# Kernel tuning notes

Measured on AMD Instinct MI355X. Metric: run time of the kernel, lower is better.

## Reference

```python
import jax, jax.numpy as jnp
import numpy as np
from jax import lax

INPUT_DIM = 256
STATE_DIM = 512
B, T = 128, 1024


def setup_inputs() -> dict:
    key = jax.random.key(0)
    ks = jax.random.split(key, 9)
    s = STATE_DIM
    i = INPUT_DIM
    # Linear(state_dim, state_dim, bias=False), weight scaled by 0.2 as in __init__
    lim_s = 1.0 / np.sqrt(s)
    lim_i = 1.0 / np.sqrt(i)
    A0_w = jax.random.uniform(ks[0], (s, s), jnp.float32, -lim_s, lim_s) * 0.2
    A1_w = jax.random.uniform(ks[1], (s, s), jnp.float32, -lim_s, lim_s) * 0.2
    B0_w = jax.random.uniform(ks[2], (s, i), jnp.float32, -lim_i, lim_i)
    B0_b = jax.random.uniform(ks[3], (s,), jnp.float32, -lim_i, lim_i)
    B1_w = jax.random.uniform(ks[4], (s, i), jnp.float32, -lim_i, lim_i)
    B1_b = jax.random.uniform(ks[5], (s,), jnp.float32, -lim_i, lim_i)
    gate_w = jax.random.uniform(ks[6], (s, i), jnp.float32, -lim_i, lim_i)
    gate_b = jax.random.uniform(ks[7], (s,), jnp.float32, -lim_i, lim_i)
    x_seq = jax.random.normal(ks[8], (B, T, i), jnp.float32)
    s0 = jnp.zeros((B, s), jnp.float32)
    alpha = jnp.float32(0.5)
    return {
        "x_seq": x_seq, "s0": s0,
        "A0_w": A0_w, "B0_w": B0_w, "B0_b": B0_b,
        "A1_w": A1_w, "B1_w": B1_w, "B1_b": B1_b,
        "gate_w": gate_w, "gate_b": gate_b,
        "alpha": alpha, "z": 1,
    }


def reference(x_seq, s0, A0_w, B0_w, B0_b, A1_w, B1_w, B1_b, gate_w, gate_b, alpha, z):
    # Precompute all input projections in one batched GEMM each: [B, T, S]
    bx0 = jnp.einsum('bti,si->bts', x_seq, B0_w) + B0_b
    bx1 = jnp.einsum('bti,si->bts', x_seq, B1_w) + B1_b
    gx = jax.nn.sigmoid(jnp.einsum('bti,si->bts', x_seq, gate_w) + gate_b)

    def step_fn(s, inputs):
        b0_t, b1_t, g_t = inputs  # each [B, S]
        f0 = jnp.tanh(s @ A0_w.T + b0_t)
        if z == 0:
            f = f0
        else:
            f1 = jnp.tanh(s @ A1_w.T + b1_t)
            f = (1.0 - alpha) * f0 + alpha * f1
        s_new = g_t * f + (1.0 - g_t) * s
        return s_new, s_new

    # scan over time: move T to leading axis
    xs = (jnp.swapaxes(bx0, 0, 1), jnp.swapaxes(bx1, 0, 1), jnp.swapaxes(gx, 0, 1))
    _, states = lax.scan(step_fn, s0, xs)  # states: [T, B, S]
    # prepend s0 -> [B, T+1, S]
    return jnp.concatenate([s0[:, None, :], jnp.swapaxes(states, 0, 1)], axis=1)
```

## Files before the change

### kernel.cpp

```cpp
#include <hip/hip_runtime.h>
#include <hip/hip_bf16.h>
#include <math.h>

typedef __attribute__((ext_vector_type(8))) short bf16x8;
typedef __attribute__((ext_vector_type(4))) float f32x4;
typedef __attribute__((ext_vector_type(4))) int i32x4;

#define TT 1024
#define BB 128
#define II 256
#define SS 512
#define OUT_T 1025
#define OUT_BSTRIDE ((size_t)OUT_T * SS)

static __device__ __forceinline__ unsigned short f2bf(float f) {
  union { float f; unsigned int u; } v; v.f = f;
  unsigned int r = v.u + 0x7fffu + ((v.u >> 16) & 1u);
  return (unsigned short)(r >> 16);
}
static __device__ __forceinline__ float bf2f(unsigned short h) {
  union { unsigned int u; float f; } v; v.u = ((unsigned int)h) << 16;
  return v.f;
}
static __device__ __forceinline__ bf16x8 pack8(const float* p) {
  float4 a = *(const float4*)p;
  float4 b = *(const float4*)(p + 4);
  bf16x8 r;
  r[0]=(short)f2bf(a.x); r[1]=(short)f2bf(a.y); r[2]=(short)f2bf(a.z); r[3]=(short)f2bf(a.w);
  r[4]=(short)f2bf(b.x); r[5]=(short)f2bf(b.y); r[6]=(short)f2bf(b.z); r[7]=(short)f2bf(b.w);
  return r;
}
static __device__ __forceinline__ float fast_tanh(float x) {
  float x2 = fminf(x * 2.8853900817779268f, 88.0f);
  float e = __builtin_amdgcn_exp2f(x2);
  return (e - 1.0f) * __builtin_amdgcn_rcpf(e + 1.0f);
}

static __device__ __forceinline__ i32x4 ld_coh_b128_issue(const void* p) {
  i32x4 r;
  asm volatile("global_load_dwordx4 %0, %1, off sc0 sc1" : "=v"(r) : "v"(p) : "memory");
  return r;
}
static __device__ __forceinline__ unsigned int ld_coh_b32(const void* p) {
  unsigned int r;
  asm volatile("global_load_dword %0, %1, off sc0 sc1\n\ts_waitcnt vmcnt(0)"
               : "=v"(r) : "v"(p) : "memory");
  return r;
}
static __device__ __forceinline__ void st_coh_b128(void* p, i32x4 v) {
  asm volatile("global_store_dwordx4 %0, %1, off sc0 sc1" :: "v"(p), "v"(v) : "memory");
}
static __device__ __forceinline__ void st_coh_b32(void* p, unsigned int v) {
  asm volatile("global_store_dword %0, %1, off sc0 sc1" :: "v"(p), "v"(v) : "memory");
}
static __device__ __forceinline__ void waitcnt_vm0() {
  asm volatile("s_waitcnt vmcnt(0)" ::: "memory");
}

__global__ __launch_bounds__(256) void proj_kernel(
    const float* __restrict__ x,
    const float* __restrict__ B0w, const float* __restrict__ B0b,
    const float* __restrict__ B1w, const float* __restrict__ B1b,
    const float* __restrict__ Gw,  const float* __restrict__ Gb,
    unsigned short* __restrict__ proj)
{
  __shared__ unsigned short Ab[64 * 40];
  __shared__ unsigned short Bb[64 * 40];
  int bid = blockIdx.x;
  int nb = bid % 24, mb = bid / 24;
  int m0 = mb * 64, n0 = nb * 64;
  const float* Wp; const float* bp; bool isgate = false;
  if (n0 < 512)       { Wp = B0w + (size_t)n0 * II;          bp = B0b + n0; }
  else if (n0 < 1024) { Wp = B1w + (size_t)(n0 - 512) * II;  bp = B1b + (n0 - 512); }
  else                { Wp = Gw  + (size_t)(n0 - 1024) * II; bp = Gb + (n0 - 1024); isgate = true; }

  int tid = threadIdx.x;
  int lane = tid & 63, wid = tid >> 6;
  int r = tid >> 2, c = tid & 3;
  int mt0 = (wid >> 1) * 2, nt0 = (wid & 1) * 2;

  f32x4 acc[2][2] = {};
  for (int k0 = 0; k0 < II; k0 += 32) {
    __syncthreads();
    *(bf16x8*)&Ab[r * 40 + c * 8] = pack8(x  + (size_t)(m0 + r) * II + k0 + c * 8);
    *(bf16x8*)&Bb[r * 40 + c * 8] = pack8(Wp + (size_t)r * II       + k0 + c * 8);
    __syncthreads();
    bf16x8 af[2], bf[2];
#pragma unroll
    for (int mi = 0; mi < 2; ++mi)
      af[mi] = *(const bf16x8*)&Ab[((mt0 + mi) * 16 + (lane & 15)) * 40 + 8 * (lane >> 4)];
#pragma unroll
    for (int ni = 0; ni < 2; ++ni)
      bf[ni] = *(const bf16x8*)&Bb[((nt0 + ni) * 16 + (lane & 15)) * 40 + 8 * (lane >> 4)];
#pragma unroll
    for (int mi = 0; mi < 2; ++mi)
#pragma unroll
      for (int ni = 0; ni < 2; ++ni)
        acc[mi][ni] = __builtin_amdgcn_mfma_f32_16x16x32_bf16(af[mi], bf[ni], acc[mi][ni], 0, 0, 0);
  }
#pragma unroll
  for (int mi = 0; mi < 2; ++mi)
#pragma unroll
    for (int ni = 0; ni < 2; ++ni)
#pragma unroll
      for (int q = 0; q < 4; ++q) {
        int m  = m0 + (mt0 + mi) * 16 + (lane >> 4) * 4 + q;
        int nl = (nt0 + ni) * 16 + (lane & 15);
        int b = m >> 10, t = m & 1023;
        float v = acc[mi][ni][q] + bp[nl];
        if (isgate) v = 1.0f / (1.0f + expf(-v));
        proj[((size_t)t * BB + b) * 1536 + n0 + nl] = f2bf(v);
      }
}

__global__ __launch_bounds__(256, 1) void recur_kernel(
    const float* __restrict__ s0,
    const float* __restrict__ A0w, const float* __restrict__ A1w,
    const unsigned short* __restrict__ proj,
    const float* __restrict__ alpha_p, const int* __restrict__ z_p,
    unsigned short* state_bf,
    unsigned int* flags,
    float* __restrict__ out)
{
  __shared__ unsigned short Ss[16 * 520];

  int tid = threadIdx.x, lane = tid & 63, wid = tid >> 6;
  int g = blockIdx.x & 7, j = blockIdx.x >> 3;
  int b0 = g * 16, c0 = j * 64;
  int lane15 = lane & 15, kslot = lane >> 4;
  int rowbase = kslot * 4;
  int colw = c0 + wid * 16 + lane15;
  float alpha = *alpha_p; int z = *z_p;
  float om_a = 1.0f - alpha;

  bf16x8 Af0[16], Af1[16];
#pragma unroll
  for (int kk = 0; kk < 16; ++kk) {
    int k0 = kk * 32 + kslot * 8;
    Af0[kk] = pack8(A0w + (size_t)colw * SS + k0);
    Af1[kk] = pack8(A1w + (size_t)colw * SS + k0);
  }

#pragma unroll
  for (int c2 = 0; c2 < 4; ++c2) {
    int e = tid + 256 * c2; int rr = e >> 6, kc = e & 63;
    *(bf16x8*)&Ss[rr * 520 + kc * 8] = pack8(s0 + (size_t)(b0 + rr) * SS + kc * 8);
  }
  if (j == 0) {
#pragma unroll
    for (int c2 = 0; c2 < 4; ++c2) {
      int e = tid + 256 * c2; int rr = e >> 6, kc = e & 63;
      const float* sp = s0 + (size_t)(b0 + rr) * SS + kc * 8;
      float* op = out + (size_t)(b0 + rr) * OUT_BSTRIDE + kc * 8;
      *(float4*)op = *(const float4*)sp;
      *(float4*)(op + 4) = *(const float4*)(sp + 4);
    }
  }
  float sprev[4];
#pragma unroll
  for (int q = 0; q < 4; ++q)
    sprev[q] = s0[(size_t)(b0 + rowbase + q) * SS + colw];

  const unsigned short* pj[4];
  unsigned short pb0[4], pb1[4], pg[4];
#pragma unroll
  for (int q = 0; q < 4; ++q) {
    pj[q] = proj + (size_t)(b0 + rowbase + q) * 1536 + colw;
    pb0[q] = pj[q][0]; pb1[q] = pj[q][512]; pg[q] = pj[q][1024];
  }

  __syncthreads();

  for (int t = 0; t < TT; ++t) {
    f32x4 acc0 = {0.f,0.f,0.f,0.f}, acc1 = {0.f,0.f,0.f,0.f};
    const unsigned short* sb = &Ss[lane15 * 520 + kslot * 8];
#pragma unroll
    for (int kk = 0; kk < 16; ++kk) {
      bf16x8 af = *(const bf16x8*)(sb + kk * 32);
      acc0 = __builtin_amdgcn_mfma_f32_16x16x32_bf16(af, Af0[kk], acc0, 0, 0, 0);
      acc1 = __builtin_amdgcn_mfma_f32_16x16x32_bf16(af, Af1[kk], acc1, 0, 0, 0);
    }
    __syncthreads();

    float sn[4];
#pragma unroll
    for (int q = 0; q < 4; ++q) {
      float f0 = fast_tanh(acc0[q] + bf2f(pb0[q]));
      float f;
      if (z != 0) {
        float f1 = fast_tanh(acc1[q] + bf2f(pb1[q]));
        f = om_a * f0 + alpha * f1;
      } else {
        f = f0;
      }
      float gg = bf2f(pg[q]);
      sn[q] = gg * f + (1.0f - gg) * sprev[q];
      sprev[q] = sn[q];
      Ss[(rowbase + q) * 520 + colw] = f2bf(sn[q]);
    }
    __syncthreads();

    unsigned short* snext = state_bf + (size_t)((t + 1) & 1) * BB * SS;
    if (tid < 128) {
      int row = tid >> 3, ch = tid & 7;
      i32x4 v = *(const i32x4*)&Ss[row * 520 + c0 + ch * 8];
      st_coh_b128(snext + (size_t)(b0 + row) * SS + c0 + ch * 8, v);
      waitcnt_vm0();
    }
    __syncthreads();
    if (tid == 0) st_coh_b32(flags + g * 8 + j, (unsigned int)(t + 1));

#pragma unroll
    for (int q = 0; q < 4; ++q)
      out[(size_t)(b0 + rowbase + q) * OUT_BSTRIDE + (size_t)(t + 1) * SS + colw] = sn[q];
    if (t + 1 < TT) {
#pragma unroll
      for (int q = 0; q < 4; ++q) {
        pj[q] += (size_t)BB * 1536;
        pb0[q] = pj[q][0]; pb1[q] = pj[q][512]; pg[q] = pj[q][1024];
      }
      if (wid == 0 && lane < 8) {
        const unsigned int* fp = flags + g * 8 + lane;
        while (ld_coh_b32(fp) < (unsigned int)(t + 1)) {}
      }
      __syncthreads();
      i32x4 v[4];
#pragma unroll
      for (int c2 = 0; c2 < 4; ++c2) {
        int e = tid + 256 * c2; int rr = e >> 6, kc = e & 63;
        v[c2] = ld_coh_b128_issue(snext + (size_t)(b0 + rr) * SS + kc * 8);
      }
      waitcnt_vm0();
#pragma unroll
      for (int c2 = 0; c2 < 4; ++c2) {
        int e = tid + 256 * c2; int rr = e >> 6, kc = e & 63;
        *(bf16x8*)&Ss[rr * 520 + kc * 8] = *(bf16x8*)&v[c2];
      }
      __syncthreads();
    }
  }
}

extern "C" void kernel_launch(void* const* d_in, const int* in_sizes, int n_in,
                              void* d_out, int out_size, void* d_ws, size_t ws_size,
                              hipStream_t stream) {
  const float* x   = (const float*)d_in[0];
  const float* s0  = (const float*)d_in[1];
  const float* A0w = (const float*)d_in[2];
  const float* B0w = (const float*)d_in[3];
  const float* B0b = (const float*)d_in[4];
  const float* A1w = (const float*)d_in[5];
  const float* B1w = (const float*)d_in[6];
  const float* B1b = (const float*)d_in[7];
  const float* Gw  = (const float*)d_in[8];
  const float* Gb  = (const float*)d_in[9];
  const float* alp = (const float*)d_in[10];
  const int*   zp  = (const int*)d_in[11];
  float* out = (float*)d_out;

  char* ws = (char*)d_ws;
  size_t proj_bytes  = (size_t)BB * TT * 1536 * 2;
  size_t state_off   = proj_bytes;
  size_t state_bytes = (size_t)2 * BB * SS * 2;
  size_t flag_off    = state_off + state_bytes;
  unsigned short* proj     = (unsigned short*)(ws);
  unsigned short* state_bf = (unsigned short*)(ws + state_off);
  unsigned int*   flags    = (unsigned int*)(ws + flag_off);

  hipMemsetAsync(flags, 0, 64 * sizeof(unsigned int), stream);

  proj_kernel<<<dim3((131072 / 64) * (1536 / 64)), dim3(256), 0, stream>>>(
      x, B0w, B0b, B1w, B1b, Gw, Gb, proj);

  recur_kernel<<<dim3(64), dim3(256), 0, stream>>>(
      s0, A0w, A1w, proj, alp, zp, state_bf, flags, out);
}
```

Before: 3.026 ms.

## Interleave two batch halves in recurrence and tile projection over all outputs per block

The recurrent kernel now runs on 32 blocks, and each block owns two 16-row batch groups. It alternates between them so that one group's state exchange and flag wait overlap the other group's MFMA compute. It also splits each accumulator into even and odd chains to shorten MFMA dependency chains, and writes the transposed MFMA output as vectorized float4 and 64-bit stores. The projection kernel keeps a 64-row x tile resident in LDS and loops over all 24 output tiles, so x is not reloaded once per tile. The cost is halving the recurrence parallelism and putting more serial work on each block.

```diff
diff --git a/kernel.cpp b/kernel.cpp
--- a/kernel.cpp
+++ b/kernel.cpp
@@ -5,6 +5,8 @@
 typedef __attribute__((ext_vector_type(8))) short bf16x8;
 typedef __attribute__((ext_vector_type(4))) float f32x4;
 typedef __attribute__((ext_vector_type(4))) int i32x4;
+typedef __attribute__((ext_vector_type(2))) int i32x2;
+typedef __attribute__((ext_vector_type(2))) unsigned int u32x2;
 
 #define TT 1024
 #define BB 128
@@ -30,6 +32,11 @@
   r[4]=(short)f2bf(b.x); r[5]=(short)f2bf(b.y); r[6]=(short)f2bf(b.z); r[7]=(short)f2bf(b.w);
   return r;
 }
+static __device__ __forceinline__ float bfat(u32x2 v, int q) {
+  unsigned int u = (q < 2) ? v[0] : v[1];
+  u = (q & 1) ? (u >> 16) : (u & 0xffffu);
+  return bf2f((unsigned short)u);
+}
 static __device__ __forceinline__ float fast_tanh(float x) {
   float x2 = fminf(x * 2.8853900817779268f, 88.0f);
   float e = __builtin_amdgcn_exp2f(x2);
@@ -47,8 +54,8 @@
                : "=v"(r) : "v"(p) : "memory");
   return r;
 }
-static __device__ __forceinline__ void st_coh_b128(void* p, i32x4 v) {
-  asm volatile("global_store_dwordx4 %0, %1, off sc0 sc1" :: "v"(p), "v"(v) : "memory");
+static __device__ __forceinline__ void st_coh_b64(void* p, i32x2 v) {
+  asm volatile("global_store_dwordx2 %0, %1, off sc0 sc1" :: "v"(p), "v"(v) : "memory");
 }
 static __device__ __forceinline__ void st_coh_b32(void* p, unsigned int v) {
   asm volatile("global_store_dword %0, %1, off sc0 sc1" :: "v"(p), "v"(v) : "memory");
@@ -64,53 +71,61 @@
     const float* __restrict__ Gw,  const float* __restrict__ Gb,
     unsigned short* __restrict__ proj)
 {
-  __shared__ unsigned short Ab[64 * 40];
-  __shared__ unsigned short Bb[64 * 40];
-  int bid = blockIdx.x;
-  int nb = bid % 24, mb = bid / 24;
-  int m0 = mb * 64, n0 = nb * 64;
-  const float* Wp; const float* bp; bool isgate = false;
-  if (n0 < 512)       { Wp = B0w + (size_t)n0 * II;          bp = B0b + n0; }
-  else if (n0 < 1024) { Wp = B1w + (size_t)(n0 - 512) * II;  bp = B1b + (n0 - 512); }
-  else                { Wp = Gw  + (size_t)(n0 - 1024) * II; bp = Gb + (n0 - 1024); isgate = true; }
-
-  int tid = threadIdx.x;
-  int lane = tid & 63, wid = tid >> 6;
-  int r = tid >> 2, c = tid & 3;
+  __shared__ unsigned short Xs[64 * 264];
+  __shared__ unsigned short Ws[64 * 40];
+
+  int m0 = blockIdx.x * 64;
+  int tid = threadIdx.x, lane = tid & 63, wid = tid >> 6;
+  int lane15 = lane & 15, kslot = lane >> 4;
   int mt0 = (wid >> 1) * 2, nt0 = (wid & 1) * 2;
-
-  f32x4 acc[2][2] = {};
-  for (int k0 = 0; k0 < II; k0 += 32) {
-    __syncthreads();
-    *(bf16x8*)&Ab[r * 40 + c * 8] = pack8(x  + (size_t)(m0 + r) * II + k0 + c * 8);
-    *(bf16x8*)&Bb[r * 40 + c * 8] = pack8(Wp + (size_t)r * II       + k0 + c * 8);
-    __syncthreads();
-    bf16x8 af[2], bf[2];
+  int sr = tid >> 2, sc = tid & 3;
+
+#pragma unroll
+  for (int it = 0; it < 8; ++it) {
+    int task = tid + 256 * it; int r = task >> 5, c = task & 31;
+    *(bf16x8*)&Xs[r * 264 + c * 8] = pack8(x + (size_t)(m0 + r) * II + c * 8);
+  }
+  __syncthreads();
+
+  for (int nt = 0; nt < 24; ++nt) {
+    int n0 = nt * 64;
+    const float* Wp; const float* bp; bool isgate = false;
+    if (n0 < 512)       { Wp = B0w + (size_t)n0 * II;          bp = B0b + n0; }
+    else if (n0 < 1024) { Wp = B1w + (size_t)(n0 - 512) * II;  bp = B1b + (n0 - 512); }
+    else                { Wp = Gw  + (size_t)(n0 - 1024) * II; bp = Gb + (n0 - 1024); isgate = true; }
+
+    f32x4 acc[2][2] = {};
+    for (int k0 = 0; k0 < II; k0 += 32) {
+      __syncthreads();
+      *(bf16x8*)&Ws[sr * 40 + sc * 8] = pack8(Wp + (size_t)sr * II + k0 + sc * 8);
+      __syncthreads();
+      bf16x8 af[2], bf[2];
+#pragma unroll
+      for (int mi = 0; mi < 2; ++mi)
+        af[mi] = *(const bf16x8*)&Xs[((mt0 + mi) * 16 + lane15) * 264 + k0 + 8 * kslot];
+#pragma unroll
+      for (int ni = 0; ni < 2; ++ni)
+        bf[ni] = *(const bf16x8*)&Ws[((nt0 + ni) * 16 + lane15) * 40 + 8 * kslot];
+#pragma unroll
+      for (int mi = 0; mi < 2; ++mi)
+#pragma unroll
+        for (int ni = 0; ni < 2; ++ni)
+          acc[mi][ni] = __builtin_amdgcn_mfma_f32_16x16x32_bf16(af[mi], bf[ni], acc[mi][ni], 0, 0, 0);
+    }
 #pragma unroll
     for (int mi = 0; mi < 2; ++mi)
-      af[mi] = *(const bf16x8*)&Ab[((mt0 + mi) * 16 + (lane & 15)) * 40 + 8 * (lane >> 4)];
-#pragma unroll
-    for (int ni = 0; ni < 2; ++ni)
-      bf[ni] = *(const bf16x8*)&Bb[((nt0 + ni) * 16 + (lane & 15)) * 40 + 8 * (lane >> 4)];
-#pragma unroll
-    for (int mi = 0; mi < 2; ++mi)
 #pragma unroll
       for (int ni = 0; ni < 2; ++ni)
-        acc[mi][ni] = __builtin_amdgcn_mfma_f32_16x16x32_bf16(af[mi], bf[ni], acc[mi][ni], 0, 0, 0);
-  }
-#pragma unroll
-  for (int mi = 0; mi < 2; ++mi)
-#pragma unroll
-    for (int ni = 0; ni < 2; ++ni)
-#pragma unroll
-      for (int q = 0; q < 4; ++q) {
-        int m  = m0 + (mt0 + mi) * 16 + (lane >> 4) * 4 + q;
-        int nl = (nt0 + ni) * 16 + (lane & 15);
-        int b = m >> 10, t = m & 1023;
-        float v = acc[mi][ni][q] + bp[nl];
-        if (isgate) v = 1.0f / (1.0f + expf(-v));
-        proj[((size_t)t * BB + b) * 1536 + n0 + nl] = f2bf(v);
-      }
+#pragma unroll
+        for (int q = 0; q < 4; ++q) {
+          int m  = m0 + (mt0 + mi) * 16 + kslot * 4 + q;
+          int nl = (nt0 + ni) * 16 + lane15;
+          int b = m >> 10, t = m & 1023;
+          float v = acc[mi][ni][q] + bp[nl];
+          if (isgate) v = 1.0f / (1.0f + expf(-v));
+          proj[((size_t)t * BB + b) * 1536 + n0 + nl] = f2bf(v);
+        }
+  }
 }
 
 __global__ __launch_bounds__(256, 1) void recur_kernel(
@@ -122,16 +137,18 @@
     unsigned int* flags,
     float* __restrict__ out)
 {
-  __shared__ unsigned short Ss[16 * 520];
+  __shared__ unsigned short SsA[16 * 520];
+  __shared__ unsigned short SsB[16 * 520];
 
   int tid = threadIdx.x, lane = tid & 63, wid = tid >> 6;
-  int g = blockIdx.x & 7, j = blockIdx.x >> 3;
-  int b0 = g * 16, c0 = j * 64;
+  int g = blockIdx.x & 3, j = blockIdx.x >> 2;
+  int bA = g * 32, bB = g * 32 + 16;
+  int c0 = j * 64;
   int lane15 = lane & 15, kslot = lane >> 4;
-  int rowbase = kslot * 4;
   int colw = c0 + wid * 16 + lane15;
-  float alpha = *alpha_p; int z = *z_p;
-  float om_a = 1.0f - alpha;
+  int ccb  = c0 + wid * 16 + kslot * 4;
+  int rowA = bA + lane15, rowB = bB + lane15;
+  float alpha = *alpha_p; int z = *z_p; float om_a = 1.0f - alpha;
 
   bf16x8 Af0[16], Af1[16];
 #pragma unroll
@@ -144,97 +161,158 @@
 #pragma unroll
   for (int c2 = 0; c2 < 4; ++c2) {
     int e = tid + 256 * c2; int rr = e >> 6, kc = e & 63;
-    *(bf16x8*)&Ss[rr * 520 + kc * 8] = pack8(s0 + (size_t)(b0 + rr) * SS + kc * 8);
+    *(bf16x8*)&SsA[rr * 520 + kc * 8] = pack8(s0 + (size_t)(bA + rr) * SS + kc * 8);
+    *(bf16x8*)&SsB[rr * 520 + kc * 8] = pack8(s0 + (size_t)(bB + rr) * SS + kc * 8);
   }
   if (j == 0) {
 #pragma unroll
-    for (int c2 = 0; c2 < 4; ++c2) {
-      int e = tid + 256 * c2; int rr = e >> 6, kc = e & 63;
-      const float* sp = s0 + (size_t)(b0 + rr) * SS + kc * 8;
-      float* op = out + (size_t)(b0 + rr) * OUT_BSTRIDE + kc * 8;
-      *(float4*)op = *(const float4*)sp;
-      *(float4*)(op + 4) = *(const float4*)(sp + 4);
-    }
-  }
-  float sprev[4];
-#pragma unroll
-  for (int q = 0; q < 4; ++q)
-    sprev[q] = s0[(size_t)(b0 + rowbase + q) * SS + colw];
-
-  const unsigned short* pj[4];
-  unsigned short pb0[4], pb1[4], pg[4];
-#pragma unroll
-  for (int q = 0; q < 4; ++q) {
-    pj[q] = proj + (size_t)(b0 + rowbase + q) * 1536 + colw;
-    pb0[q] = pj[q][0]; pb1[q] = pj[q][512]; pg[q] = pj[q][1024];
-  }
+    for (int it = 0; it < 16; ++it) {
+      int task = tid + 256 * it;
+      int rr = task >> 7, f4 = task & 127;
+      *(float4*)(out + (size_t)(bA + rr) * OUT_BSTRIDE + f4 * 4) =
+          *(const float4*)(s0 + (size_t)(bA + rr) * SS + f4 * 4);
+    }
+  }
+  float4 spA4 = *(const float4*)(s0 + (size_t)rowA * SS + ccb);
+  float4 spB4 = *(const float4*)(s0 + (size_t)rowB * SS + ccb);
+  float sprevA[4] = {spA4.x, spA4.y, spA4.z, spA4.w};
+  float sprevB[4] = {spB4.x, spB4.y, spB4.z, spB4.w};
+
+  const unsigned short* ppA = proj + (size_t)rowA * 1536 + ccb;
+  const unsigned short* ppB = proj + (size_t)rowB * 1536 + ccb;
+  u32x2 pA0 = *(const u32x2*)(ppA);
+  u32x2 pA1 = *(const u32x2*)(ppA + 512);
+  u32x2 pAg = *(const u32x2*)(ppA + 1024);
+  u32x2 pB0 = *(const u32x2*)(ppB);
+  u32x2 pB1 = *(const u32x2*)(ppB + 512);
+  u32x2 pBg = *(const u32x2*)(ppB + 1024);
+
+  unsigned int* flagA = flags + g * 8;
+  unsigned int* flagB = flags + 32 + g * 8;
 
   __syncthreads();
 
   for (int t = 0; t < TT; ++t) {
-    f32x4 acc0 = {0.f,0.f,0.f,0.f}, acc1 = {0.f,0.f,0.f,0.f};
-    const unsigned short* sb = &Ss[lane15 * 520 + kslot * 8];
-#pragma unroll
-    for (int kk = 0; kk < 16; ++kk) {
-      bf16x8 af = *(const bf16x8*)(sb + kk * 32);
-      acc0 = __builtin_amdgcn_mfma_f32_16x16x32_bf16(af, Af0[kk], acc0, 0, 0, 0);
-      acc1 = __builtin_amdgcn_mfma_f32_16x16x32_bf16(af, Af1[kk], acc1, 0, 0, 0);
-    }
-    __syncthreads();
-
-    float sn[4];
-#pragma unroll
-    for (int q = 0; q < 4; ++q) {
-      float f0 = fast_tanh(acc0[q] + bf2f(pb0[q]));
-      float f;
-      if (z != 0) {
-        float f1 = fast_tanh(acc1[q] + bf2f(pb1[q]));
-        f = om_a * f0 + alpha * f1;
-      } else {
-        f = f0;
-      }
-      float gg = bf2f(pg[q]);
-      sn[q] = gg * f + (1.0f - gg) * sprev[q];
-      sprev[q] = sn[q];
-      Ss[(rowbase + q) * 520 + colw] = f2bf(sn[q]);
-    }
-    __syncthreads();
-
     unsigned short* snext = state_bf + (size_t)((t + 1) & 1) * BB * SS;
-    if (tid < 128) {
-      int row = tid >> 3, ch = tid & 7;
-      i32x4 v = *(const i32x4*)&Ss[row * 520 + c0 + ch * 8];
-      st_coh_b128(snext + (size_t)(b0 + row) * SS + c0 + ch * 8, v);
+
+    {
+      f32x4 a0e = {}, a0o = {}, a1e = {}, a1o = {};
+      const unsigned short* sb = &SsA[lane15 * 520 + kslot * 8];
+#pragma unroll
+      for (int kk = 0; kk < 16; kk += 2) {
+        bf16x8 f0 = *(const bf16x8*)(sb + kk * 32);
+        bf16x8 f1 = *(const bf16x8*)(sb + (kk + 1) * 32);
+        a0e = __builtin_amdgcn_mfma_f32_16x16x32_bf16(Af0[kk],     f0, a0e, 0, 0, 0);
+        a1e = __builtin_amdgcn_mfma_f32_16x16x32_bf16(Af1[kk],     f0, a1e, 0, 0, 0);
+        a0o = __builtin_amdgcn_mfma_f32_16x16x32_bf16(Af0[kk + 1], f1, a0o, 0, 0, 0);
+        a1o = __builtin_amdgcn_mfma_f32_16x16x32_bf16(Af1[kk + 1], f1, a1o, 0, 0, 0);
+      }
+      float snA[4];
+#pragma unroll
+      for (int q = 0; q < 4; ++q) {
+        float f0 = fast_tanh((a0e[q] + a0o[q]) + bfat(pA0, q));
+        float f;
+        if (z != 0) {
+          float f1 = fast_tanh((a1e[q] + a1o[q]) + bfat(pA1, q));
+          f = om_a * f0 + alpha * f1;
+        } else f = f0;
+        float gg = bfat(pAg, q);
+        snA[q] = gg * f + (1.0f - gg) * sprevA[q];
+        sprevA[q] = snA[q];
+      }
+      float4 o4 = {snA[0], snA[1], snA[2], snA[3]};
+      *(float4*)(out + (size_t)rowA * OUT_BSTRIDE + (size_t)(t + 1) * SS + ccb) = o4;
+      i32x2 w;
+      w[0] = (int)(((unsigned)f2bf(snA[0])) | (((unsigned)f2bf(snA[1])) << 16));
+      w[1] = (int)(((unsigned)f2bf(snA[2])) | (((unsigned)f2bf(snA[3])) << 16));
+      st_coh_b64(snext + (size_t)rowA * SS + ccb, w);
       waitcnt_vm0();
-    }
-    __syncthreads();
-    if (tid == 0) st_coh_b32(flags + g * 8 + j, (unsigned int)(t + 1));
-
-#pragma unroll
-    for (int q = 0; q < 4; ++q)
-      out[(size_t)(b0 + rowbase + q) * OUT_BSTRIDE + (size_t)(t + 1) * SS + colw] = sn[q];
-    if (t + 1 < TT) {
-#pragma unroll
-      for (int q = 0; q < 4; ++q) {
-        pj[q] += (size_t)BB * 1536;
-        pb0[q] = pj[q][0]; pb1[q] = pj[q][512]; pg[q] = pj[q][1024];
-      }
-      if (wid == 0 && lane < 8) {
-        const unsigned int* fp = flags + g * 8 + lane;
-        while (ld_coh_b32(fp) < (unsigned int)(t + 1)) {}
-      }
-      __syncthreads();
+      __syncthreads();
+      if (tid == 0) st_coh_b32(flagA + j, (unsigned int)(t + 1));
+      if (t + 1 < TT) {
+        ppA += (size_t)BB * 1536;
+        pA0 = *(const u32x2*)(ppA);
+        pA1 = *(const u32x2*)(ppA + 512);
+        pAg = *(const u32x2*)(ppA + 1024);
+      }
+    }
+
+    if (t > 0) {
+      if (tid < 8) { while (ld_coh_b32(flagB + tid) < (unsigned int)t) {} }
+      __syncthreads();
+      const unsigned short* sbg = state_bf + (size_t)(t & 1) * BB * SS + (size_t)bB * SS;
       i32x4 v[4];
 #pragma unroll
       for (int c2 = 0; c2 < 4; ++c2) {
         int e = tid + 256 * c2; int rr = e >> 6, kc = e & 63;
-        v[c2] = ld_coh_b128_issue(snext + (size_t)(b0 + rr) * SS + kc * 8);
+        v[c2] = ld_coh_b128_issue(sbg + rr * SS + kc * 8);
       }
       waitcnt_vm0();
 #pragma unroll
       for (int c2 = 0; c2 < 4; ++c2) {
         int e = tid + 256 * c2; int rr = e >> 6, kc = e & 63;
-        *(bf16x8*)&Ss[rr * 520 + kc * 8] = *(bf16x8*)&v[c2];
+        *(bf16x8*)&SsB[rr * 520 + kc * 8] = *(bf16x8*)&v[c2];
+      }
+      __syncthreads();
+    }
+
+    {
+      f32x4 a0e = {}, a0o = {}, a1e = {}, a1o = {};
+      const unsigned short* sb = &SsB[lane15 * 520 + kslot * 8];
+#pragma unroll
+      for (int kk = 0; kk < 16; kk += 2) {
+        bf16x8 f0 = *(const bf16x8*)(sb + kk * 32);
+        bf16x8 f1 = *(const bf16x8*)(sb + (kk + 1) * 32);
+        a0e = __builtin_amdgcn_mfma_f32_16x16x32_bf16(Af0[kk],     f0, a0e, 0, 0, 0);
+        a1e = __builtin_amdgcn_mfma_f32_16x16x32_bf16(Af1[kk],     f0, a1e, 0, 0, 0);
+        a0o = __builtin_amdgcn_mfma_f32_16x16x32_bf16(Af0[kk + 1], f1, a0o, 0, 0, 0);
+        a1o = __builtin_amdgcn_mfma_f32_16x16x32_bf16(Af1[kk + 1], f1, a1o, 0, 0, 0);
+      }
+      float snB[4];
+#pragma unroll
+      for (int q = 0; q < 4; ++q) {
+        float f0 = fast_tanh((a0e[q] + a0o[q]) + bfat(pB0, q));
+        float f;
+        if (z != 0) {
+          float f1 = fast_tanh((a1e[q] + a1o[q]) + bfat(pB1, q));
+          f = om_a * f0 + alpha * f1;
+        } else f = f0;
+        float gg = bfat(pBg, q);
+        snB[q] = gg * f + (1.0f - gg) * sprevB[q];
+        sprevB[q] = snB[q];
+      }
+      float4 o4 = {snB[0], snB[1], snB[2], snB[3]};
+      *(float4*)(out + (size_t)rowB * OUT_BSTRIDE + (size_t)(t + 1) * SS + ccb) = o4;
+      i32x2 w;
+      w[0] = (int)(((unsigned)f2bf(snB[0])) | (((unsigned)f2bf(snB[1])) << 16));
+      w[1] = (int)(((unsigned)f2bf(snB[2])) | (((unsigned)f2bf(snB[3])) << 16));
+      st_coh_b64(snext + (size_t)rowB * SS + ccb, w);
+      waitcnt_vm0();
+      __syncthreads();
+      if (tid == 0) st_coh_b32(flagB + j, (unsigned int)(t + 1));
+      if (t + 1 < TT) {
+        ppB += (size_t)BB * 1536;
+        pB0 = *(const u32x2*)(ppB);
+        pB1 = *(const u32x2*)(ppB + 512);
+        pBg = *(const u32x2*)(ppB + 1024);
+      }
+    }
+
+    if (t + 1 < TT) {
+      if (tid < 8) { while (ld_coh_b32(flagA + tid) < (unsigned int)(t + 1)) {} }
+      __syncthreads();
+      const unsigned short* sbg = state_bf + (size_t)((t + 1) & 1) * BB * SS + (size_t)bA * SS;
+      i32x4 v[4];
+#pragma unroll
+      for (int c2 = 0; c2 < 4; ++c2) {
+        int e = tid + 256 * c2; int rr = e >> 6, kc = e & 63;
+        v[c2] = ld_coh_b128_issue(sbg + rr * SS + kc * 8);
+      }
+      waitcnt_vm0();
+#pragma unroll
+      for (int c2 = 0; c2 < 4; ++c2) {
+        int e = tid + 256 * c2; int rr = e >> 6, kc = e & 63;
+        *(bf16x8*)&SsA[rr * 520 + kc * 8] = *(bf16x8*)&v[c2];
       }
       __syncthreads();
     }
@@ -269,9 +347,9 @@
 
   hipMemsetAsync(flags, 0, 64 * sizeof(unsigned int), stream);
 
-  proj_kernel<<<dim3((131072 / 64) * (1536 / 64)), dim3(256), 0, stream>>>(
+  proj_kernel<<<dim3(131072 / 64), dim3(256), 0, stream>>>(
       x, B0w, B0b, B1w, B1b, Gw, Gb, proj);
 
-  recur_kernel<<<dim3(64), dim3(256), 0, stream>>>(
+  recur_kernel<<<dim3(32), dim3(256), 0, stream>>>(
       s0, A0w, A1w, proj, alp, zp, state_bf, flags, out);
 }
```

Result: slower. 5.672 ms (+87.4%).

## Replace flag barrier with tagged per-word state exchange and restage projection GEMM

Applied to the files above, without the earlier changes.

The recurrence kernel drops the separate flag array and the store/wait/flag/poll sequence. Each state word now carries its bf16 value in the high half and a 16-bit timestep tag in the low half, so consumers poll the data itself and no longer need a flag barrier. State is double-buffered in LDS, fewer block barriers are used per step, MFMA accumulation is split into even and odd chains, and outputs are written with vector stores. The projection kernel now keeps a 64-row X tile resident in LDS and loops over all 24 N tiles, avoiding repeated x loads and conversions. The tag check relies on 128-bit coherent loads being atomic per word and on the 16-bit tag not wrapping.

```diff
diff --git a/kernel.cpp b/kernel.cpp
--- a/kernel.cpp
+++ b/kernel.cpp
@@ -5,6 +5,7 @@
 typedef __attribute__((ext_vector_type(8))) short bf16x8;
 typedef __attribute__((ext_vector_type(4))) float f32x4;
 typedef __attribute__((ext_vector_type(4))) int i32x4;
+typedef __attribute__((ext_vector_type(2))) unsigned int u32x2;
 
 #define TT 1024
 #define BB 128
@@ -30,6 +31,11 @@
   r[4]=(short)f2bf(b.x); r[5]=(short)f2bf(b.y); r[6]=(short)f2bf(b.z); r[7]=(short)f2bf(b.w);
   return r;
 }
+static __device__ __forceinline__ float bfat(u32x2 v, int q) {
+  unsigned int u = (q < 2) ? v[0] : v[1];
+  u = (q & 1) ? (u >> 16) : (u & 0xffffu);
+  return bf2f((unsigned short)u);
+}
 static __device__ __forceinline__ float fast_tanh(float x) {
   float x2 = fminf(x * 2.8853900817779268f, 88.0f);
   float e = __builtin_amdgcn_exp2f(x2);
@@ -41,17 +47,8 @@
   asm volatile("global_load_dwordx4 %0, %1, off sc0 sc1" : "=v"(r) : "v"(p) : "memory");
   return r;
 }
-static __device__ __forceinline__ unsigned int ld_coh_b32(const void* p) {
-  unsigned int r;
-  asm volatile("global_load_dword %0, %1, off sc0 sc1\n\ts_waitcnt vmcnt(0)"
-               : "=v"(r) : "v"(p) : "memory");
-  return r;
-}
 static __device__ __forceinline__ void st_coh_b128(void* p, i32x4 v) {
   asm volatile("global_store_dwordx4 %0, %1, off sc0 sc1" :: "v"(p), "v"(v) : "memory");
-}
-static __device__ __forceinline__ void st_coh_b32(void* p, unsigned int v) {
-  asm volatile("global_store_dword %0, %1, off sc0 sc1" :: "v"(p), "v"(v) : "memory");
 }
 static __device__ __forceinline__ void waitcnt_vm0() {
   asm volatile("s_waitcnt vmcnt(0)" ::: "memory");
@@ -64,53 +61,61 @@
     const float* __restrict__ Gw,  const float* __restrict__ Gb,
     unsigned short* __restrict__ proj)
 {
-  __shared__ unsigned short Ab[64 * 40];
-  __shared__ unsigned short Bb[64 * 40];
-  int bid = blockIdx.x;
-  int nb = bid % 24, mb = bid / 24;
-  int m0 = mb * 64, n0 = nb * 64;
-  const float* Wp; const float* bp; bool isgate = false;
-  if (n0 < 512)       { Wp = B0w + (size_t)n0 * II;          bp = B0b + n0; }
-  else if (n0 < 1024) { Wp = B1w + (size_t)(n0 - 512) * II;  bp = B1b + (n0 - 512); }
-  else                { Wp = Gw  + (size_t)(n0 - 1024) * II; bp = Gb + (n0 - 1024); isgate = true; }
-
-  int tid = threadIdx.x;
-  int lane = tid & 63, wid = tid >> 6;
-  int r = tid >> 2, c = tid & 3;
+  __shared__ unsigned short Xs[64 * 264];
+  __shared__ unsigned short Ws[64 * 40];
+
+  int m0 = blockIdx.x * 64;
+  int tid = threadIdx.x, lane = tid & 63, wid = tid >> 6;
+  int lane15 = lane & 15, kslot = lane >> 4;
   int mt0 = (wid >> 1) * 2, nt0 = (wid & 1) * 2;
-
-  f32x4 acc[2][2] = {};
-  for (int k0 = 0; k0 < II; k0 += 32) {
-    __syncthreads();
-    *(bf16x8*)&Ab[r * 40 + c * 8] = pack8(x  + (size_t)(m0 + r) * II + k0 + c * 8);
-    *(bf16x8*)&Bb[r * 40 + c * 8] = pack8(Wp + (size_t)r * II       + k0 + c * 8);
-    __syncthreads();
-    bf16x8 af[2], bf[2];
+  int sr = tid >> 2, sc = tid & 3;
+
+#pragma unroll
+  for (int it = 0; it < 8; ++it) {
+    int task = tid + 256 * it; int r = task >> 5, c = task & 31;
+    *(bf16x8*)&Xs[r * 264 + c * 8] = pack8(x + (size_t)(m0 + r) * II + c * 8);
+  }
+  __syncthreads();
+
+  for (int nt = 0; nt < 24; ++nt) {
+    int n0 = nt * 64;
+    const float* Wp; const float* bp; bool isgate = false;
+    if (n0 < 512)       { Wp = B0w + (size_t)n0 * II;          bp = B0b + n0; }
+    else if (n0 < 1024) { Wp = B1w + (size_t)(n0 - 512) * II;  bp = B1b + (n0 - 512); }
+    else                { Wp = Gw  + (size_t)(n0 - 1024) * II; bp = Gb + (n0 - 1024); isgate = true; }
+
+    f32x4 acc[2][2] = {};
+    for (int k0 = 0; k0 < II; k0 += 32) {
+      __syncthreads();
+      *(bf16x8*)&Ws[sr * 40 + sc * 8] = pack8(Wp + (size_t)sr * II + k0 + sc * 8);
+      __syncthreads();
+      bf16x8 af[2], bf[2];
+#pragma unroll
+      for (int mi = 0; mi < 2; ++mi)
+        af[mi] = *(const bf16x8*)&Xs[((mt0 + mi) * 16 + lane15) * 264 + k0 + 8 * kslot];
+#pragma unroll
+      for (int ni = 0; ni < 2; ++ni)
+        bf[ni] = *(const bf16x8*)&Ws[((nt0 + ni) * 16 + lane15) * 40 + 8 * kslot];
+#pragma unroll
+      for (int mi = 0; mi < 2; ++mi)
+#pragma unroll
+        for (int ni = 0; ni < 2; ++ni)
+          acc[mi][ni] = __builtin_amdgcn_mfma_f32_16x16x32_bf16(af[mi], bf[ni], acc[mi][ni], 0, 0, 0);
+    }
 #pragma unroll
     for (int mi = 0; mi < 2; ++mi)
-      af[mi] = *(const bf16x8*)&Ab[((mt0 + mi) * 16 + (lane & 15)) * 40 + 8 * (lane >> 4)];
-#pragma unroll
-    for (int ni = 0; ni < 2; ++ni)
-      bf[ni] = *(const bf16x8*)&Bb[((nt0 + ni) * 16 + (lane & 15)) * 40 + 8 * (lane >> 4)];
-#pragma unroll
-    for (int mi = 0; mi < 2; ++mi)
 #pragma unroll
       for (int ni = 0; ni < 2; ++ni)
-        acc[mi][ni] = __builtin_amdgcn_mfma_f32_16x16x32_bf16(af[mi], bf[ni], acc[mi][ni], 0, 0, 0);
-  }
-#pragma unroll
-  for (int mi = 0; mi < 2; ++mi)
-#pragma unroll
-    for (int ni = 0; ni < 2; ++ni)
-#pragma unroll
-      for (int q = 0; q < 4; ++q) {
-        int m  = m0 + (mt0 + mi) * 16 + (lane >> 4) * 4 + q;
-        int nl = (nt0 + ni) * 16 + (lane & 15);
-        int b = m >> 10, t = m & 1023;
-        float v = acc[mi][ni][q] + bp[nl];
-        if (isgate) v = 1.0f / (1.0f + expf(-v));
-        proj[((size_t)t * BB + b) * 1536 + n0 + nl] = f2bf(v);
-      }
+#pragma unroll
+        for (int q = 0; q < 4; ++q) {
+          int m  = m0 + (mt0 + mi) * 16 + kslot * 4 + q;
+          int nl = (nt0 + ni) * 16 + lane15;
+          int b = m >> 10, t = m & 1023;
+          float v = acc[mi][ni][q] + bp[nl];
+          if (isgate) v = 1.0f / (1.0f + expf(-v));
+          proj[((size_t)t * BB + b) * 1536 + n0 + nl] = f2bf(v);
+        }
+  }
 }
 
 __global__ __launch_bounds__(256, 1) void recur_kernel(
@@ -118,125 +123,130 @@
     const float* __restrict__ A0w, const float* __restrict__ A1w,
     const unsigned short* __restrict__ proj,
     const float* __restrict__ alpha_p, const int* __restrict__ z_p,
-    unsigned short* state_bf,
-    unsigned int* flags,
+    unsigned int* state32,
     float* __restrict__ out)
 {
-  __shared__ unsigned short Ss[16 * 520];
+  __shared__ unsigned short Sbuf[2][16 * 520];
 
   int tid = threadIdx.x, lane = tid & 63, wid = tid >> 6;
   int g = blockIdx.x & 7, j = blockIdx.x >> 3;
   int b0 = g * 16, c0 = j * 64;
   int lane15 = lane & 15, kslot = lane >> 4;
-  int rowbase = kslot * 4;
-  int colw = c0 + wid * 16 + lane15;
-  float alpha = *alpha_p; int z = *z_p;
-  float om_a = 1.0f - alpha;
+  int colA = c0 + wid * 16 + lane15;
+  int ccb  = c0 + wid * 16 + kslot * 4;
+  int row  = b0 + lane15;
+  int prow = tid >> 4, pch = tid & 15;
+  float alpha = *alpha_p; int z = *z_p; float om_a = 1.0f - alpha;
 
   bf16x8 Af0[16], Af1[16];
 #pragma unroll
   for (int kk = 0; kk < 16; ++kk) {
     int k0 = kk * 32 + kslot * 8;
-    Af0[kk] = pack8(A0w + (size_t)colw * SS + k0);
-    Af1[kk] = pack8(A1w + (size_t)colw * SS + k0);
+    Af0[kk] = pack8(A0w + (size_t)colA * SS + k0);
+    Af1[kk] = pack8(A1w + (size_t)colA * SS + k0);
   }
 
 #pragma unroll
   for (int c2 = 0; c2 < 4; ++c2) {
     int e = tid + 256 * c2; int rr = e >> 6, kc = e & 63;
-    *(bf16x8*)&Ss[rr * 520 + kc * 8] = pack8(s0 + (size_t)(b0 + rr) * SS + kc * 8);
+    *(bf16x8*)&Sbuf[0][rr * 520 + kc * 8] = pack8(s0 + (size_t)(b0 + rr) * SS + kc * 8);
   }
   if (j == 0) {
 #pragma unroll
-    for (int c2 = 0; c2 < 4; ++c2) {
-      int e = tid + 256 * c2; int rr = e >> 6, kc = e & 63;
-      const float* sp = s0 + (size_t)(b0 + rr) * SS + kc * 8;
-      float* op = out + (size_t)(b0 + rr) * OUT_BSTRIDE + kc * 8;
-      *(float4*)op = *(const float4*)sp;
-      *(float4*)(op + 4) = *(const float4*)(sp + 4);
-    }
-  }
-  float sprev[4];
-#pragma unroll
-  for (int q = 0; q < 4; ++q)
-    sprev[q] = s0[(size_t)(b0 + rowbase + q) * SS + colw];
-
-  const unsigned short* pj[4];
-  unsigned short pb0[4], pb1[4], pg[4];
-#pragma unroll
-  for (int q = 0; q < 4; ++q) {
-    pj[q] = proj + (size_t)(b0 + rowbase + q) * 1536 + colw;
-    pb0[q] = pj[q][0]; pb1[q] = pj[q][512]; pg[q] = pj[q][1024];
-  }
+    for (int it = 0; it < 8; ++it) {
+      int task = tid + 256 * it;
+      int rr = task >> 7, f4 = task & 127;
+      *(float4*)(out + (size_t)(b0 + rr) * OUT_BSTRIDE + f4 * 4) =
+          *(const float4*)(s0 + (size_t)(b0 + rr) * SS + f4 * 4);
+    }
+  }
+  float4 sp4 = *(const float4*)(s0 + (size_t)row * SS + ccb);
+  float sprev[4] = {sp4.x, sp4.y, sp4.z, sp4.w};
+
+  const unsigned short* pp = proj + (size_t)row * 1536 + ccb;
+  u32x2 pb0 = *(const u32x2*)(pp);
+  u32x2 pb1 = *(const u32x2*)(pp + 512);
+  u32x2 pg  = *(const u32x2*)(pp + 1024);
 
   __syncthreads();
 
   for (int t = 0; t < TT; ++t) {
-    f32x4 acc0 = {0.f,0.f,0.f,0.f}, acc1 = {0.f,0.f,0.f,0.f};
-    const unsigned short* sb = &Ss[lane15 * 520 + kslot * 8];
-#pragma unroll
-    for (int kk = 0; kk < 16; ++kk) {
-      bf16x8 af = *(const bf16x8*)(sb + kk * 32);
-      acc0 = __builtin_amdgcn_mfma_f32_16x16x32_bf16(af, Af0[kk], acc0, 0, 0, 0);
-      acc1 = __builtin_amdgcn_mfma_f32_16x16x32_bf16(af, Af1[kk], acc1, 0, 0, 0);
-    }
-    __syncthreads();
+    int par = t & 1;
+
+    if (t > 0) {
+      const unsigned int* sb = state32 + (size_t)par * BB * SS + (size_t)(b0 + prow) * SS;
+      unsigned int expd = (unsigned int)t;
+      i32x4 v[7];
+#pragma unroll
+      for (int s = 0; s < 7; ++s) {
+        int p = s + (s >= j ? 1 : 0);
+        v[s] = ld_coh_b128_issue(sb + p * 64 + pch * 4);
+      }
+      waitcnt_vm0();
+#pragma unroll
+      for (int s = 0; s < 7; ++s) {
+        int p = s + (s >= j ? 1 : 0);
+        while (((((unsigned)v[s][0] ^ expd) | ((unsigned)v[s][1] ^ expd) |
+                 ((unsigned)v[s][2] ^ expd) | ((unsigned)v[s][3] ^ expd)) & 0xffffu) != 0u) {
+          v[s] = ld_coh_b128_issue(sb + p * 64 + pch * 4);
+          waitcnt_vm0();
+        }
+        unsigned int d0 = ((unsigned)v[s][0] >> 16) | ((unsigned)v[s][1] & 0xffff0000u);
+        unsigned int d1 = ((unsigned)v[s][2] >> 16) | ((unsigned)v[s][3] & 0xffff0000u);
+        u32x2 dd; dd[0] = d0; dd[1] = d1;
+        *(u32x2*)&Sbuf[par][prow * 520 + p * 64 + pch * 4] = dd;
+      }
+      __syncthreads();
+    }
+
+    f32x4 a0e = {}, a0o = {}, a1e = {}, a1o = {};
+    const unsigned short* sb = &Sbuf[par][lane15 * 520 + kslot * 8];
+#pragma unroll
+    for (int kk = 0; kk < 16; kk += 2) {
+      bf16x8 f0 = *(const bf16x8*)(sb + kk * 32);
+      bf16x8 f1 = *(const bf16x8*)(sb + (kk + 1) * 32);
+      a0e = __builtin_amdgcn_mfma_f32_16x16x32_bf16(Af0[kk],     f0, a0e, 0, 0, 0);
+      a1e = __builtin_amdgcn_mfma_f32_16x16x32_bf16(Af1[kk],     f0, a1e, 0, 0, 0);
+      a0o = __builtin_amdgcn_mfma_f32_16x16x32_bf16(Af0[kk + 1], f1, a0o, 0, 0, 0);
+      a1o = __builtin_amdgcn_mfma_f32_16x16x32_bf16(Af1[kk + 1], f1, a1o, 0, 0, 0);
+    }
 
     float sn[4];
 #pragma unroll
     for (int q = 0; q < 4; ++q) {
-      float f0 = fast_tanh(acc0[q] + bf2f(pb0[q]));
+      float f0 = fast_tanh((a0e[q] + a0o[q]) + bfat(pb0, q));
       float f;
       if (z != 0) {
-        float f1 = fast_tanh(acc1[q] + bf2f(pb1[q]));
+        float f1 = fast_tanh((a1e[q] + a1o[q]) + bfat(pb1, q));
         f = om_a * f0 + alpha * f1;
-      } else {
-        f = f0;
-      }
-      float gg = bf2f(pg[q]);
+      } else f = f0;
+      float gg = bfat(pg, q);
       sn[q] = gg * f + (1.0f - gg) * sprev[q];
       sprev[q] = sn[q];
-      Ss[(rowbase + q) * 520 + colw] = f2bf(sn[q]);
-    }
-    __syncthreads();
-
-    unsigned short* snext = state_bf + (size_t)((t + 1) & 1) * BB * SS;
-    if (tid < 128) {
-      int row = tid >> 3, ch = tid & 7;
-      i32x4 v = *(const i32x4*)&Ss[row * 520 + c0 + ch * 8];
-      st_coh_b128(snext + (size_t)(b0 + row) * SS + c0 + ch * 8, v);
-      waitcnt_vm0();
-    }
-    __syncthreads();
-    if (tid == 0) st_coh_b32(flags + g * 8 + j, (unsigned int)(t + 1));
-
-#pragma unroll
-    for (int q = 0; q < 4; ++q)
-      out[(size_t)(b0 + rowbase + q) * OUT_BSTRIDE + (size_t)(t + 1) * SS + colw] = sn[q];
+    }
+
+    {
+      u32x2 dd;
+      dd[0] = (unsigned)f2bf(sn[0]) | ((unsigned)f2bf(sn[1]) << 16);
+      dd[1] = (unsigned)f2bf(sn[2]) | ((unsigned)f2bf(sn[3]) << 16);
+      *(u32x2*)&Sbuf[par ^ 1][lane15 * 520 + ccb] = dd;
+    }
+    {
+      i32x4 w;
+#pragma unroll
+      for (int q = 0; q < 4; ++q)
+        w[q] = (int)(((unsigned)f2bf(sn[q]) << 16) | (unsigned)(t + 1));
+      st_coh_b128(state32 + (size_t)((t + 1) & 1) * BB * SS + (size_t)row * SS + ccb, w);
+    }
+    {
+      float4 o4 = {sn[0], sn[1], sn[2], sn[3]};
+      *(float4*)(out + (size_t)row * OUT_BSTRIDE + (size_t)(t + 1) * SS + ccb) = o4;
+    }
     if (t + 1 < TT) {
-#pragma unroll
-      for (int q = 0; q < 4; ++q) {
-        pj[q] += (size_t)BB * 1536;
-        pb0[q] = pj[q][0]; pb1[q] = pj[q][512]; pg[q] = pj[q][1024];
-      }
-      if (wid == 0 && lane < 8) {
-        const unsigned int* fp = flags + g * 8 + lane;
-        while (ld_coh_b32(fp) < (unsigned int)(t + 1)) {}
-      }
-      __syncthreads();
-      i32x4 v[4];
-#pragma unroll
-      for (int c2 = 0; c2 < 4; ++c2) {
-        int e = tid + 256 * c2; int rr = e >> 6, kc = e & 63;
-        v[c2] = ld_coh_b128_issue(snext + (size_t)(b0 + rr) * SS + kc * 8);
-      }
-      waitcnt_vm0();
-#pragma unroll
-      for (int c2 = 0; c2 < 4; ++c2) {
-        int e = tid + 256 * c2; int rr = e >> 6, kc = e & 63;
-        *(bf16x8*)&Ss[rr * 520 + kc * 8] = *(bf16x8*)&v[c2];
-      }
-      __syncthreads();
+      pp += (size_t)BB * 1536;
+      pb0 = *(const u32x2*)(pp);
+      pb1 = *(const u32x2*)(pp + 512);
+      pg  = *(const u32x2*)(pp + 1024);
     }
   }
 }
@@ -259,19 +269,15 @@
   float* out = (float*)d_out;
 
   char* ws = (char*)d_ws;
-  size_t proj_bytes  = (size_t)BB * TT * 1536 * 2;
-  size_t state_off   = proj_bytes;
-  size_t state_bytes = (size_t)2 * BB * SS * 2;
-  size_t flag_off    = state_off + state_bytes;
-  unsigned short* proj     = (unsigned short*)(ws);
-  unsigned short* state_bf = (unsigned short*)(ws + state_off);
-  unsigned int*   flags    = (unsigned int*)(ws + flag_off);
-
-  hipMemsetAsync(flags, 0, 64 * sizeof(unsigned int), stream);
-
-  proj_kernel<<<dim3((131072 / 64) * (1536 / 64)), dim3(256), 0, stream>>>(
+  size_t proj_bytes = (size_t)BB * TT * 1536 * 2;
+  unsigned short* proj    = (unsigned short*)(ws);
+  unsigned int*   state32 = (unsigned int*)(ws + proj_bytes);
+
+  hipMemsetAsync(state32, 0, (size_t)2 * BB * SS * 4, stream);
+
+  proj_kernel<<<dim3(131072 / 64), dim3(256), 0, stream>>>(
       x, B0w, B0b, B1w, B1b, Gw, Gb, proj);
 
   recur_kernel<<<dim3(64), dim3(256), 0, stream>>>(
-      s0, A0w, A1w, proj, alp, zp, state_bf, flags, out);
-}
+      s0, A0w, A1w, proj, alp, zp, state32, out);
+}
```

Result: slower. 3.201 ms (+5.8%).
